# Optimization experiments

Measured on AMD Instinct MI355X. Metric: run time of the kernel, lower is better.

Reference implementation:

```python
import jax, jax.numpy as jnp
import numpy as np
import math

DEPTH = 3
HID = 32


def _dense_adj(edge_index, n, dtype):
    # scatter edges into dense adjacency, drop self-loops (gcn_norm re-adds them)
    A = jnp.zeros((n, n), dtype).at[edge_index[0], edge_index[1]].add(1.0)
    return A * (1.0 - jnp.eye(n, dtype=dtype))


def _gcn(x, A, W, b):
    # GCNConv(improved=True): self-loop weight 2.0, symmetric deg normalization
    n = A.shape[0]
    Ah = A + 2.0 * jnp.eye(n, dtype=x.dtype)
    deg = Ah.sum(axis=1)
    d = jnp.where(deg > 0, jax.lax.rsqrt(deg), 0.0)
    An = d[:, None] * Ah * d[None, :]
    return An @ (x @ W) + b


def _augment(A):
    # GraphUNet.augment_adj: add self loops, A @ A, remove self loops
    n = A.shape[0]
    Ai = A + jnp.eye(n, dtype=A.dtype)
    A2 = Ai @ Ai
    return A2 * (1.0 - jnp.eye(n, dtype=A.dtype))


def _topk_pool(x, A, p, k):
    # TopKPooling: score = tanh(x.p/||p||), keep top-k, scale kept features
    score = jnp.tanh((x @ p) / jnp.linalg.norm(p))
    _, perm = jax.lax.top_k(score, k)
    xp = x[perm] * score[perm][:, None]
    Ap = A[perm][:, perm]
    return xp, Ap, perm


def _graph_unet(x, edge_index, Ws, bs, Us, ubs, ps):
    n = x.shape[0]
    ratios = [2000.0 / n, 0.5, 0.5]
    A = _dense_adj(edge_index, n, x.dtype)
    x = jax.nn.relu(_gcn(x, A, Ws[0], bs[0]))
    xs, As, perms = [x], [A], []
    for i in range(1, DEPTH + 1):
        A = _augment(A)
        k = math.ceil(ratios[i - 1] * x.shape[0])  # static shapes: 2000,1000,500
        x, A, perm = _topk_pool(x, A, ps[i - 1], k)
        x = jax.nn.relu(_gcn(x, A, Ws[i], bs[i]))
        if i < DEPTH:
            xs.append(x)
            As.append(A)
        perms.append(perm)
    for i in range(DEPTH):
        j = DEPTH - 1 - i
        res, A, perm = xs[j], As[j], perms[j]
        up = jnp.zeros_like(res).at[perm].set(x)
        x = _gcn(res + up, A, Us[i], ubs[i])
        if i < DEPTH - 1:
            x = jax.nn.relu(x)
    return x


def setup_inputs() -> dict:
    key = jax.random.key(0)
    N, F_IN, C, E = 4096, 1433, 16, 131072
    ks = jax.random.split(key, 20)
    inp = {
        "x": jax.random.normal(ks[0], (N, F_IN), jnp.float32),
        "edge_index": jax.random.randint(ks[1], (2, E), 0, N, jnp.int64),
    }
    inp["W0"] = jax.random.normal(ks[2], (F_IN, HID), jnp.float32) * 0.05
    inp["b0"] = jnp.zeros((HID,), jnp.float32)
    for i in range(1, 4):
        inp[f"W{i}"] = jax.random.normal(ks[2 + i], (HID, HID), jnp.float32) * 0.1
        inp[f"b{i}"] = jnp.zeros((HID,), jnp.float32)
    inp["U0"] = jax.random.normal(ks[6], (HID, HID), jnp.float32) * 0.1
    inp["c0"] = jnp.zeros((HID,), jnp.float32)
    inp["U1"] = jax.random.normal(ks[7], (HID, HID), jnp.float32) * 0.1
    inp["c1"] = jnp.zeros((HID,), jnp.float32)
    inp["U2"] = jax.random.normal(ks[8], (HID, C), jnp.float32) * 0.1
    inp["c2"] = jnp.zeros((C,), jnp.float32)
    # TopKPooling score vectors
    for i in range(3):
        inp[f"p{i}"] = jax.random.normal(ks[9 + i], (HID,), jnp.float32)
    return inp


def reference(x, edge_index, W0, b0, W1, b1, W2, b2, W3, b3,
              U0, c0, U1, c1, U2, c2, p0, p1, p2):
    # eval mode: dropout_adj and F.dropout are identity
    Ws = [W0, W1, W2, W3]
    bs = [b0, b1, b2, b3]
    Us = [U0, U1, U2]
    ubs = [c0, c1, c2]
    ps = [p0, p1, p2]
    out = _graph_unet(x, edge_index, Ws, bs, Us, ubs, ps)
    return jax.nn.log_softmax(out, axis=1)
```

## Files before the change

### kernel.cpp

```cpp
#include <hip/hip_runtime.h>
#include <math.h>
#include <stddef.h>

#define N0   4096
#define NE   131072
#define FIN  1433
#define HID  32
#define NCLS 16
#define KP1  2000
#define KP2  1000
#define KP3  500
#define RCH  512

typedef __attribute__((ext_vector_type(8))) short bf16x8;
typedef __attribute__((ext_vector_type(4))) float f32x4;


__global__ __launch_bounds__(256) void k_fill0_u32(unsigned* p, size_t n) {
    size_t i = (size_t)blockIdx.x * blockDim.x + threadIdx.x;
    size_t st = (size_t)gridDim.x * blockDim.x;
    for (; i < n; i += st) p[i] = 0u;
}

__global__ __launch_bounds__(256) void k_scatter2c(const int* ei, unsigned* A0w, unsigned* A0Tw, int* ecnt) {
    int e = blockIdx.x * blockDim.x + threadIdx.x;
    if (e >= NE) return;
    int r = ei[e], c = ei[NE + e];
    if (r == c) return;
    size_t idx = (size_t)r * N0 + c;
    atomicAdd(&A0w[idx >> 2], 1u << (8 * (idx & 3)));
    size_t idt = (size_t)c * N0 + r;
    atomicAdd(&A0Tw[idt >> 2], 1u << (8 * (idt & 3)));
    atomicAdd(&ecnt[r], 1);
}

__global__ __launch_bounds__(256) void k_dvec(const int* ecnt, float* dv, int n) {
    int i = blockIdx.x * blockDim.x + threadIdx.x;
    if (i < n) dv[i] = (float)(1.0 / sqrt((double)ecnt[i] + 2.0));
}

__global__ __launch_bounds__(256) void k_scan1(const int* __restrict__ d, int* __restrict__ o) {
    __shared__ int buf[N0];
    __shared__ int part[256];
    int tid = threadIdx.x;
    for (int t = tid; t < N0; t += 256) buf[t] = d[t];
    __syncthreads();
    int base = tid * (N0 / 256);
    int s = 0;
    #pragma unroll
    for (int j = 0; j < N0 / 256; j++) s += buf[base + j];
    part[tid] = s;
    __syncthreads();
    for (int offd = 1; offd < 256; offd <<= 1) {
        int v = (tid >= offd) ? part[tid - offd] : 0;
        __syncthreads();
        part[tid] += v;
        __syncthreads();
    }
    int run = (tid == 0) ? 0 : part[tid - 1];
    #pragma unroll
    for (int j = 0; j < N0 / 256; j++) {
        int tmp = buf[base + j];
        o[base + j] = run;
        run += tmp;
    }
}

__global__ __launch_bounds__(256) void k_fillout(const int* ei, const int* outoff, int* ocur, int* outlist) {
    int e = blockIdx.x * 256 + threadIdx.x;
    if (e >= NE) return;
    int u = ei[e], v = ei[NE + e];
    if (u == v) return;
    int s = atomicAdd(&ocur[u], 1);
    outlist[outoff[u] + s] = v;
}

__global__ __launch_bounds__(256) void k_fcount(const int* ei, const int* rk, int* focnt) {
    int e = blockIdx.x * 256 + threadIdx.x;
    if (e >= NE) return;
    int u = ei[e], v = ei[NE + e];
    if (u == v) return;
    if (rk[v] < KP1) atomicAdd(&focnt[u], 1);
}

__global__ __launch_bounds__(256) void k_ffill(const int* ei, const int* rk, const int* foutoff,
                                               int* fcur, int* foutlist) {
    int e = blockIdx.x * 256 + threadIdx.x;
    if (e >= NE) return;
    int u = ei[e], v = ei[NE + e];
    if (u == v) return;
    int rv = rk[v];
    if (rv >= KP1) return;
    int s = atomicAdd(&fcur[u], 1);
    foutlist[foutoff[u] + s] = rv;
}

__global__ __launch_bounds__(256) void k_spaug2(const int* __restrict__ ecnt, const int* __restrict__ outoff,
                                                const int* __restrict__ outlist,
                                                const int* __restrict__ focnt, const int* __restrict__ foutoff,
                                                const int* __restrict__ foutlist,
                                                const int* __restrict__ perm,
                                                float* __restrict__ A1, float* __restrict__ dv1) {
    __shared__ float rowacc[KP1];
    __shared__ float red[256];
    int r1 = blockIdx.x, tid = threadIdx.x;
    for (int j = tid; j < KP1; j += 256) rowacc[j] = 0.f;
    int pr1 = perm[r1];
    __syncthreads();
    int od = ecnt[pr1], ob = outoff[pr1];
    for (int ki = tid; ki < od; ki += 256) {
        int k = outlist[ob + ki];
        int fb = foutoff[k], fc = focnt[k];
        for (int j = 0; j < fc; j++) atomicAdd(&rowacc[foutlist[fb + j]], 1.f);
    }
    {
        int fb = foutoff[pr1], fc = focnt[pr1];
        for (int j = tid; j < fc; j += 256) atomicAdd(&rowacc[foutlist[fb + j]], 2.f);
    }
    __syncthreads();
    if (tid == 0) rowacc[r1] = 0.f;
    __syncthreads();
    float rs = 0.f;
    for (int j = tid * 4; j < KP1; j += 1024) {
        float4 v = *(const float4*)&rowacc[j];
        rs += v.x + v.y + v.z + v.w;
        *(float4*)&A1[(size_t)r1 * KP1 + j] = v;
    }
    red[tid] = rs; __syncthreads();
    for (int o = 128; o > 0; o >>= 1) {
        if (tid < o) red[tid] += red[tid + o];
        __syncthreads();
    }
    if (tid == 0) dv1[r1] = (float)(1.0 / sqrt((double)red[0] + 2.0));
}

__global__ __launch_bounds__(256) void k_degf(const float* A, int n, float* dv) {
    int i = blockIdx.x;
    const float* row = A + (size_t)i * n;
    float acc = 0.f;
    for (int j = threadIdx.x * 4; j < n; j += 256 * 4) {
        float4 w = *(const float4*)&row[j];
        acc += w.x + w.y + w.z + w.w;
    }
    __shared__ float red[256];
    red[threadIdx.x] = acc; __syncthreads();
    for (int off = 128; off > 0; off >>= 1) {
        if (threadIdx.x < off) red[threadIdx.x] += red[threadIdx.x + off];
        __syncthreads();
    }
    if (threadIdx.x == 0) dv[i] = (float)(1.0 / sqrt((double)red[0] + 2.0));
}

template <int NC>
__global__ __launch_bounds__(256) void k_xw2(const float* __restrict__ X, const float* __restrict__ W,
                                             const float* __restrict__ dvv, float* __restrict__ YB,
                                             int M, int K,
                                             const float* __restrict__ UP, const int* __restrict__ rkl, int kup) {
    constexpr int BR = 256 / NC;
    constexpr int BK = 64;
    constexpr int XEL = BR * BK / 256;
    constexpr int WEL = BK * NC / 256;
    __shared__ float Xs[BR][BK + 4];
    __shared__ float Ws[BK][NC];
    int r0 = blockIdx.x * BR;
    int tid = threadIdx.x;
    int c = tid % NC, r = tid / NC;
    int xli = tid * XEL, xr = xli / BK, xc = xli % BK;
    int wli = tid * WEL, wk = wli / NC, wc = wli % NC;
    int grow = r0 + xr;
    int upr = -1;
    if (UP && grow < M) { int rr = rkl[grow]; if (rr < kup) upr = rr; }
    float acc = 0.f;

    for (int k0 = 0; k0 < K; k0 += BK) {
        __syncthreads();
        #pragma unroll
        for (int e = 0; e < XEL; e++) {
            int kk = k0 + xc + e;
            float v = (grow < M && kk < K) ? X[(size_t)grow * K + kk] : 0.f;
            if (upr >= 0 && kk < K) v += UP[(size_t)upr * K + kk];
            Xs[xr][xc + e] = v;
        }
        if (k0 + wk < K) {
            #pragma unroll
            for (int e = 0; e < WEL; e += 4)
                *(float4*)&Ws[wk][wc + e] = *(const float4*)&W[(size_t)(k0 + wk) * NC + wc + e];
        } else {
            #pragma unroll
            for (int e = 0; e < WEL; e++) Ws[wk][wc + e] = 0.f;
        }
        __syncthreads();
        #pragma unroll 8
        for (int k = 0; k < BK; k++) acc += Xs[r][k] * Ws[k][c];
    }
    int orow = r0 + r;
    if (orow < M) YB[(size_t)orow * NC + c] = dvv[orow] * acc;
}

__global__ __launch_bounds__(256) void k_xw2sk(const float* __restrict__ X, const float* __restrict__ W,
                                               float* __restrict__ xwp, int M, int K, int chunk) {
    constexpr int NC = 32, BR = 8, BK = 64;
    __shared__ float Xs[BR][BK + 4];
    __shared__ float Ws[BK][NC];
    int r0 = blockIdx.x * BR;
    int s  = blockIdx.y;
    int kb = s * chunk, ke = min(kb + chunk, K);
    int tid = threadIdx.x;
    int c = tid % NC, r = tid / NC;
    int xli = tid * 2, xr = xli / BK, xc = xli % BK;
    int wli = tid * 8, wk = wli / NC, wc = wli % NC;
    int grow = r0 + xr;
    float acc = 0.f;

    for (int k0 = kb; k0 < ke; k0 += BK) {
        __syncthreads();
        #pragma unroll
        for (int e = 0; e < 2; e++) {
            int kk = k0 + xc + e;
            Xs[xr][xc + e] = (grow < M && kk < K) ? X[(size_t)grow * K + kk] : 0.f;
        }
        if (k0 + wk < K) {
            #pragma unroll
            for (int e = 0; e < 8; e += 4)
                *(float4*)&Ws[wk][wc + e] = *(const float4*)&W[(size_t)(k0 + wk) * NC + wc + e];
        } else {
            #pragma unroll
            for (int e = 0; e < 8; e++) Ws[wk][wc + e] = 0.f;
        }
        __syncthreads();
        #pragma unroll 8
        for (int k = 0; k < BK; k++) acc += Xs[r][k] * Ws[k][c];
    }
    int orow = r0 + r;
    if (orow < M) xwp[((size_t)s * M + orow) * NC + c] = acc;
}

__global__ __launch_bounds__(256) void k_xwred(const float* __restrict__ xwp, int S,
                                               const float* __restrict__ dvv, float* __restrict__ yb, int M) {
    int idx = blockIdx.x * 256 + threadIdx.x;
    if (idx >= M * 32) return;
    float s = 0.f;
    for (int t = 0; t < S; t++) s += xwp[(size_t)t * M * 32 + idx];
    yb[idx] = dvv[idx / 32] * s;
}


template <class T, int NC>
__global__ __launch_bounds__(256) void k_agg(const T* __restrict__ A, const float* __restrict__ y,
                                             float* __restrict__ part, int n, int M, int chunk) {
    constexpr int G   = 256 / NC;
    constexpr int RPT = 64 / G;
    __shared__ float At[64][72];
    __shared__ float ys[64][NC];
    int r0 = blockIdx.x * 64;
    int s  = blockIdx.y;
    int k_begin = s * chunk;
    int k_end   = min(k_begin + chunk, n);
    int tid = threadIdx.x;
    int c = tid % NC, g = tid / NC;
    int r = tid & 63, kq = tid >> 6;
    bool row_ok = (r0 + r) < M;
    float acc[RPT] = {};

    for (int k0 = k_begin; k0 < k_end; k0 += 64) {
        __syncthreads();
        if constexpr (sizeof(T) == 1) {
            uint4 w = {0u, 0u, 0u, 0u};
            if (row_ok) w = *(const uint4*)&A[(size_t)(r0 + r) * n + k0 + kq * 16];
            #pragma unroll
            for (int j = 0; j < 16; j++) {
                int kl = kq * 16 + j;
                unsigned b = (((const unsigned*)&w)[j >> 2] >> (8 * (j & 3))) & 0xffu;
                At[kl][r] = (k0 + kl < k_end) ? (float)b : 0.f;
            }
        } else {
            #pragma unroll
            for (int q = 0; q < 4; q++) {
                int kl = kq * 16 + q * 4;
                float4 w = {0.f, 0.f, 0.f, 0.f};
                if (row_ok) w = *(const float4*)&A[(size_t)(r0 + r) * n + k0 + kl];
                At[kl + 0][r] = (k0 + kl + 0 < k_end) ? w.x : 0.f;
                At[kl + 1][r] = (k0 + kl + 1 < k_end) ? w.y : 0.f;
                At[kl + 2][r] = (k0 + kl + 2 < k_end) ? w.z : 0.f;
                At[kl + 3][r] = (k0 + kl + 3 < k_end) ? w.w : 0.f;
            }
        }
        constexpr int NF4 = 64 * NC / 4;
        #pragma unroll
        for (int f = 0; f < NF4 / 256; f++) {
            int fi = tid + f * 256;
            int k = fi / (NC / 4), cb = fi % (NC / 4);
            float4 w = *(const float4*)&y[(size_t)(k0 + k) * NC + cb * 4];
            *(float4*)&ys[k][cb * 4] = w;
        }
        __syncthreads();
        for (int k = 0; k < 64; k++) {
            float yv = ys[k][c];
            #pragma unroll
            for (int i = 0; i < RPT; i += 4) {
                float4 a = *(const float4*)&At[k][g * RPT + i];
                acc[i + 0] += a.x * yv;
                acc[i + 1] += a.y * yv;
                acc[i + 2] += a.z * yv;
                acc[i + 3] += a.w * yv;
            }
        }
    }
    #pragma unroll
    for (int i = 0; i < RPT; i++) {
        int row = r0 + g * RPT + i;
        if (row < M) part[((size_t)s * M + row) * NC + c] = acc[i];
    }
}

template <int NC>
__global__ __launch_bounds__(256) void k_aggfin(const float* __restrict__ part, int S,
                                                const float* __restrict__ y, const float* __restrict__ dvv,
                                                const float* __restrict__ bias, float* __restrict__ out,
                                                int M, int relu) {
    int idx = blockIdx.x * blockDim.x + threadIdx.x;
    if (idx >= M * NC) return;
    int i = idx / NC, c = idx % NC;
    float sum = 0.f;
    for (int s = 0; s < S; s++) sum += part[(size_t)s * M * NC + idx];
    float di = dvv[i];
    float v = di * sum + 2.f * di * y[idx] + bias[c];
    if (relu) v = fmaxf(v, 0.f);
    out[idx] = v;
}

__global__ __launch_bounds__(256) void k_aggfin_lsm(const float* __restrict__ part, int S,
                                                    const float* __restrict__ y, const float* __restrict__ dvv,
                                                    const float* __restrict__ bias, float* __restrict__ out,
                                                    int M) {
    __shared__ float vv[16][NCLS + 1];
    int idx = blockIdx.x * 256 + threadIdx.x;
    int i = idx / NCLS, c = idx % NCLS;
    int lr = threadIdx.x / NCLS;
    float v = 0.f;
    if (i < M) {
        float sum = 0.f;
        for (int s = 0; s < S; s++) sum += part[(size_t)s * M * NCLS + idx];
        float di = dvv[i];
        v = di * sum + 2.f * di * y[idx] + bias[c];
    }
    vv[lr][c] = v;
    __syncthreads();
    if (i >= M) return;
    float m = -1e30f;
    for (int cc = 0; cc < NCLS; cc++) m = fmaxf(m, vv[lr][cc]);
    float se = 0.f;
    for (int cc = 0; cc < NCLS; cc++) se += expf(vv[lr][cc] - m);
    float ls = logf(se);
    out[idx] = v - m - ls;
}


__global__ __launch_bounds__(256) void k_rankscore(const float* __restrict__ x, const float* __restrict__ p,
                                                   int* __restrict__ rk, int n) {
    __shared__ float sj[RCH];
    float pv[HID];
    #pragma unroll
    for (int c = 0; c < HID; c++) pv[c] = p[c];
    float nrm = 0.f;
    #pragma unroll
    for (int c = 0; c < HID; c++) nrm += pv[c] * pv[c];
    nrm = sqrtf(nrm);
    int jb = blockIdx.y * RCH;
    int len = min(jb + RCH, n) - jb;
    for (int t = threadIdx.x; t < len; t += 256) {
        const float* xr = x + (size_t)(jb + t) * HID;
        float d = 0.f;
        #pragma unroll
        for (int c = 0; c < HID; c++) d += xr[c] * pv[c];
        sj[t] = tanhf(d / nrm);
    }
    __syncthreads();
    int i = blockIdx.x * 256 + threadIdx.x;
    if (i >= n) return;
    const float* xi = x + (size_t)i * HID;
    float di = 0.f;
    #pragma unroll
    for (int c = 0; c < HID; c++) di += xi[c] * pv[c];
    float si = tanhf(di / nrm);
    int r = 0;
    for (int j = 0; j < len; j += 4) {
        float4 v = *(const float4*)&sj[j];
        int jg = jb + j;
        r += (v.x > si) || (v.x == si && (jg + 0) < i);
        r += (v.y > si) || (v.y == si && (jg + 1) < i);
        r += (v.z > si) || (v.z == si && (jg + 2) < i);
        r += (v.w > si) || (v.w == si && (jg + 3) < i);
    }
    atomicAdd(&rk[i], r);
}

__global__ __launch_bounds__(256) void k_permpool2(const float* __restrict__ x, const float* __restrict__ p,
                                                   const int* __restrict__ rk, int* __restrict__ perm,
                                                   float* __restrict__ xp, int n, int k) {
    int i = blockIdx.x * 256 + threadIdx.x;
    if (i >= n) return;
    int r = rk[i];
    if (r >= k) return;
    perm[r] = i;
    float pv[HID];
    #pragma unroll
    for (int c = 0; c < HID; c++) pv[c] = p[c];
    float nrm = 0.f;
    #pragma unroll
    for (int c = 0; c < HID; c++) nrm += pv[c] * pv[c];
    nrm = sqrtf(nrm);
    const float* xi = x + (size_t)i * HID;
    float d = 0.f;
    #pragma unroll
    for (int c = 0; c < HID; c++) d += xi[c] * pv[c];
    float si = tanhf(d / nrm);
    const float4* xr = (const float4*)xi;
    float4* xpo = (float4*)(xp + (size_t)r * HID);
    #pragma unroll
    for (int c = 0; c < HID / 4; c++) {
        float4 v = xr[c];
        v.x *= si; v.y *= si; v.z *= si; v.w *= si;
        xpo[c] = v;
    }
}


template <class T>
__global__ __launch_bounds__(256) void k_gcols(const T* A, const int* perm, T* CG, int n, int kk) {
    size_t idx = (size_t)blockIdx.x * blockDim.x + threadIdx.x;
    if (idx >= (size_t)n * kk) return;
    int k = (int)(idx / kk), r2 = (int)(idx % kk);
    int pc = perm[r2];
    T v = A[(size_t)k * n + pc];
    if (k == pc) v = (T)(v + (T)1);
    CG[idx] = v;
}

__global__ __launch_bounds__(256) void k_gemm_pool_sk(const float* A, const int* perm, const float* CG,
                                                      float* part, int n, int kk, int chunk) {
    __shared__ float As[16][65];
    __shared__ float Bs[16][65];
    __shared__ int   pr[64];
    int r0 = blockIdx.y * 64, c0 = blockIdx.x * 64;
    int s  = blockIdx.z;
    int k_begin = s * chunk;
    int k_end   = min(k_begin + chunk, n);
    int tx = threadIdx.x % 16, ty = threadIdx.x / 16;

    for (int t = threadIdx.x; t < 64; t += 256) {
        int rg = r0 + t;
        pr[t] = (rg < kk) ? perm[rg] : -1;
    }
    __syncthreads();

    float acc[4][4] = {};
    int cB = threadIdx.x % 64, kB = threadIdx.x / 64;

    for (int k0 = k_begin; k0 < k_end; k0 += 16) {
        for (int pass = 0; pass < 4; pass++) {
            int rr = ty + pass * 16;
            int kk_ = k0 + tx;
            int prow = pr[rr];
            float v = 0.f;
            if (prow >= 0 && kk_ < k_end) {
                v = A[(size_t)prow * n + kk_];
                if (prow == kk_) v += 1.f;
            }
            As[tx][rr] = v;
        }
        for (int pass = 0; pass < 4; pass++) {
            int k = kB + 4 * pass;
            int cg = c0 + cB;
            float v = 0.f;
            if (cg < kk && (k0 + k) < k_end) v = CG[(size_t)(k0 + k) * kk + cg];
            Bs[k][cB] = v;
        }
        __syncthreads();
        for (int k = 0; k < 16; k++) {
            float a[4], b[4];
            #pragma unroll
            for (int i = 0; i < 4; i++) a[i] = As[k][ty * 4 + i];
            #pragma unroll
            for (int j = 0; j < 4; j++) b[j] = Bs[k][tx * 4 + j];
            #pragma unroll
            for (int i = 0; i < 4; i++)
                #pragma unroll
                for (int j = 0; j < 4; j++) acc[i][j] += a[i] * b[j];
        }
        __syncthreads();
    }
    for (int i = 0; i < 4; i++) {
        int rg = r0 + ty * 4 + i;
        if (rg >= kk) continue;
        for (int j = 0; j < 4; j++) {
            int cg = c0 + tx * 4 + j;
            if (cg >= kk) continue;
            part[((size_t)s * kk + rg) * kk + cg] = acc[i][j];
        }
    }
}

__global__ __launch_bounds__(256) void k_gpfin(const float* __restrict__ part, int S, float* __restrict__ Ap, int kk) {
    int idx = blockIdx.x * blockDim.x + threadIdx.x;
    if (idx >= kk * kk) return;
    int rg = idx / kk, cg = idx % kk;
    float sum = 0.f;
    for (int s = 0; s < S; s++) sum += part[(size_t)s * kk * kk + idx];
    Ap[idx] = (rg == cg) ? 0.f : sum;
}


__global__ __launch_bounds__(256) void k_tr_f32(const float* A, float* AT, int n) {
    __shared__ float t[32][33];
    int bx = blockIdx.x * 32, by = blockIdx.y * 32;
    int tx = threadIdx.x % 32, ty = threadIdx.x / 32;
    for (int p = 0; p < 4; p++) {
        int r = by + ty + p * 8, c = bx + tx;
        t[ty + p * 8][tx] = (r < n && c < n) ? A[(size_t)r * n + c] : 0.f;
    }
    __syncthreads();
    for (int p = 0; p < 4; p++) {
        int r = bx + ty + p * 8, c = by + tx;
        if (r < n && c < n) AT[(size_t)r * n + c] = t[tx][ty + p * 8];
    }
}

__global__ __launch_bounds__(256) void k_prepfb(const float* A, const float* AT,
                                                int n, int Kpad, const int* perm, int kk,
                                                unsigned short* dstA, unsigned short* dstB) {
    const float* src = blockIdx.y ? AT : A;
    unsigned short* dst = blockIdx.y ? dstB : dstA;
    int r = blockIdx.x;
    unsigned short* drow = dst + (size_t)r * Kpad;
    if (r >= kk) {
        for (int k = threadIdx.x; k < Kpad; k += 256) drow[k] = 0;
        return;
    }
    int pr = perm[r];
    const float* srow = src + (size_t)pr * n;
    for (int k = threadIdx.x; k < Kpad; k += 256) {
        float v = (k < n) ? srow[k] : 0.f;
        if (k == pr) v += 1.f;
        drow[k] = (unsigned short)(__float_as_uint(v) >> 16);
    }
}

__global__ __launch_bounds__(512) void k_mfma_pool(const unsigned short* Abf, const unsigned short* Bbf,
                                                   float* Ap, int Kpad, int kk, int chunk) {
    __shared__ short As[128 * 64];
    __shared__ short Bs[128 * 64];
    int r0 = blockIdx.y * 128, c0 = blockIdx.x * 128;
    int z0 = blockIdx.z * chunk;
    int tid = threadIdx.x;
    int l = tid & 63, w = tid >> 6;
    int wm = w >> 2, wn = w & 3;
    f32x4 acc[4][2] = {};

    for (int k0 = z0; k0 < z0 + chunk; k0 += 64) {
        __syncthreads();
        #pragma unroll
        for (int p = 0; p < 2; p++) {
            int row = p * 64 + (tid >> 3);
            int ch  = tid & 7;
            int byte = row * 128 + ((ch * 16) ^ ((row & 7) << 4));
            bf16x8 va = *(const bf16x8*)&Abf[(size_t)(r0 + row) * Kpad + k0 + ch * 8];
            *(bf16x8*)((char*)As + byte) = va;
            bf16x8 vb = *(const bf16x8*)&Bbf[(size_t)(c0 + row) * Kpad + k0 + ch * 8];
            *(bf16x8*)((char*)Bs + byte) = vb;
        }
        __syncthreads();
        #pragma unroll
        for (int h = 0; h < 2; h++) {
            bf16x8 af[4], bfr[2];
            #pragma unroll
            for (int i = 0; i < 4; i++) {
                int row = wm * 64 + i * 16 + (l & 15);
                int byte = row * 128 + ((h * 64 + (l >> 4) * 16) ^ ((row & 7) << 4));
                af[i] = *(const bf16x8*)((const char*)As + byte);
            }
            #pragma unroll
            for (int j = 0; j < 2; j++) {
                int row = wn * 32 + j * 16 + (l & 15);
                int byte = row * 128 + ((h * 64 + (l >> 4) * 16) ^ ((row & 7) << 4));
                bfr[j] = *(const bf16x8*)((const char*)Bs + byte);
            }
            #pragma unroll
            for (int i = 0; i < 4; i++)
                #pragma unroll
                for (int j = 0; j < 2; j++)
                    acc[i][j] = __builtin_amdgcn_mfma_f32_16x16x32_bf16(af[i], bfr[j], acc[i][j], 0, 0, 0);
        }
    }
    #pragma unroll
    for (int i = 0; i < 4; i++) {
        #pragma unroll
        for (int j = 0; j < 2; j++) {
            int cg = c0 + wn * 32 + j * 16 + (l & 15);
            if (cg < kk) {
                #pragma unroll
                for (int q = 0; q < 4; q++) {
                    int rg = r0 + wm * 64 + i * 16 + (l >> 4) * 4 + q;
                    if (rg < kk && rg != cg) atomicAdd(&Ap[(size_t)rg * kk + cg], acc[i][j][q]);
                }
            }
        }
    }
}


extern "C" void kernel_launch(void* const* d_in, const int* in_sizes, int n_in,
                              void* d_out, int out_size, void* d_ws, size_t ws_size,
                              hipStream_t stream) {
    const float* x  = (const float*)d_in[0];
    const int*   ei = (const int*)d_in[1];
    const float* W0 = (const float*)d_in[2];  const float* b0 = (const float*)d_in[3];
    const float* W1 = (const float*)d_in[4];  const float* b1 = (const float*)d_in[5];
    const float* W2 = (const float*)d_in[6];  const float* b2 = (const float*)d_in[7];
    const float* W3 = (const float*)d_in[8];  const float* b3 = (const float*)d_in[9];
    const float* U0 = (const float*)d_in[10]; const float* c0 = (const float*)d_in[11];
    const float* U1 = (const float*)d_in[12]; const float* c1 = (const float*)d_in[13];
    const float* U2 = (const float*)d_in[14]; const float* c2 = (const float*)d_in[15];
    const float* p0 = (const float*)d_in[16];
    const float* p1 = (const float*)d_in[17];
    const float* p2 = (const float*)d_in[18];
    float* out = (float*)d_out;

    char* w = (char*)d_ws;
    size_t off = 0;
    auto alloc = [&](size_t bytes) -> void* {
        void* p = w + off;
        off += (bytes + 255) / 256 * 256;
        return p;
    };
    unsigned char* A0u = (unsigned char*)alloc((size_t)N0 * N0);
    unsigned char* A0T = (unsigned char*)alloc((size_t)N0 * N0);
    int*   ecnt = (int*)alloc((size_t)N0 * 4);
    int*   ocur = (int*)alloc((size_t)N0 * 4);
    int*   focnt = (int*)alloc((size_t)N0 * 4);
    int*   fcur  = (int*)alloc((size_t)N0 * 4);
    float* A1  = (float*)alloc((size_t)KP1 * KP1 * 4);
    float* A1T = (float*)alloc((size_t)KP1 * KP1 * 4);
    float* A2  = (float*)alloc((size_t)KP2 * KP2 * 4);
    float* A3  = (float*)alloc((size_t)KP3 * KP3 * 4);
    float* CG  = (float*)alloc((size_t)KP2 * KP3 * 4);
    unsigned short* Abf = (unsigned short*)alloc((size_t)2048 * 4096 * 2);
    unsigned short* Bbf = (unsigned short*)alloc((size_t)2048 * 4096 * 2);
    float* part = (float*)alloc((size_t)4 * N0 * HID * 4);
    float* x0  = (float*)alloc((size_t)N0 * HID * 4);
    float* x1  = (float*)alloc((size_t)KP1 * HID * 4);
    float* x2  = (float*)alloc((size_t)KP2 * HID * 4);
    float* x3  = (float*)alloc((size_t)KP3 * HID * 4);
    float* xp  = (float*)alloc((size_t)KP1 * HID * 4);
    float* ua  = (float*)alloc((size_t)KP2 * HID * 4);
    float* ub  = (float*)alloc((size_t)KP1 * HID * 4);
    float* yb  = (float*)alloc((size_t)N0 * HID * 4);
    float* dv0 = (float*)alloc((size_t)N0 * 4);
    float* dv1 = (float*)alloc((size_t)KP1 * 4);
    float* dv2 = (float*)alloc((size_t)KP2 * 4);
    float* dv3 = (float*)alloc((size_t)KP3 * 4);
    int*   rkA = (int*)alloc((size_t)N0 * 4);
    int*   rkB = (int*)alloc((size_t)KP1 * 4);
    int*   rkC = (int*)alloc((size_t)KP2 * 4);
    int*   pm0 = (int*)alloc((size_t)KP1 * 4);
    int*   pm1 = (int*)alloc((size_t)KP2 * 4);
    int*   pm2 = (int*)alloc((size_t)KP3 * 4);
    int*   outoff  = (int*)alloc((size_t)N0 * 4);
    int*   foutoff = (int*)alloc((size_t)N0 * 4);
    int*   outlist  = (int*)alloc((size_t)NE * 4);
    int*   foutlist = (int*)alloc((size_t)NE * 4);
    (void)ws_size; (void)in_sizes; (void)n_in; (void)out_size;

    auto gcn_f = [&](const float* A, int n, const float* xin, int K, const float* W,
                     const float* bias, const float* dvv, int relu, float* outv, int S, int chunk,
                     const float* UP, const int* rkl, int kup) {
        k_xw2<32><<<(n + 7) / 8, 256, 0, stream>>>(xin, W, dvv, yb, n, K, UP, rkl, kup);
        dim3 g((n + 63) / 64, S);
        k_agg<float, 32><<<g, 256, 0, stream>>>(A, yb, part, n, n, chunk);
        k_aggfin<32><<<(n * 32 + 255) / 256, 256, 0, stream>>>(part, S, yb, dvv, bias, outv, n, relu);
    };
    auto pool = [&](const float* xin, const float* p, int n, int k, int* rkbuf, int* perm, float* xpo) {
        k_fill0_u32<<<16, 256, 0, stream>>>((unsigned*)rkbuf, (size_t)n);
        dim3 gr((n + 255) / 256, (n + RCH - 1) / RCH);
        k_rankscore<<<gr, 256, 0, stream>>>(xin, p, rkbuf, n);
        k_permpool2<<<(n + 255) / 256, 256, 0, stream>>>(xin, p, rkbuf, perm, xpo, n, k);
    };

    k_fill0_u32<<<2048, 256, 0, stream>>>((unsigned*)A0u, ((size_t)2 * N0 * N0 + (size_t)4 * N0 * 4) / 4);
    k_scatter2c<<<(NE + 255) / 256, 256, 0, stream>>>(ei, (unsigned*)A0u, (unsigned*)A0T, ecnt);
    k_dvec<<<16, 256, 0, stream>>>(ecnt, dv0, N0);
    k_scan1<<<1, 256, 0, stream>>>(ecnt, outoff);
    k_fillout<<<(NE + 255) / 256, 256, 0, stream>>>(ei, outoff, ocur, outlist);

    k_xw2sk<<<dim3(N0 / 8, 4), 256, 0, stream>>>(x, W0, part, N0, FIN, 384);
    k_xwred<<<(N0 * 32 + 255) / 256, 256, 0, stream>>>(part, 4, dv0, yb, N0);
    {
        dim3 g((N0 + 63) / 64, 4);
        k_agg<unsigned char, 32><<<g, 256, 0, stream>>>(A0u, yb, part, N0, N0, 1024);
        k_aggfin<32><<<(N0 * 32 + 255) / 256, 256, 0, stream>>>(part, 4, yb, dv0, b0, x0, N0, 1);
    }
    pool(x0, p0, N0, KP1, rkA, pm0, xp);

    k_fcount<<<(NE + 255) / 256, 256, 0, stream>>>(ei, rkA, focnt);
    k_scan1<<<1, 256, 0, stream>>>(focnt, foutoff);
    k_ffill<<<(NE + 255) / 256, 256, 0, stream>>>(ei, rkA, foutoff, fcur, foutlist);
    k_spaug2<<<KP1, 256, 0, stream>>>(ecnt, outoff, outlist, focnt, foutoff, foutlist, pm0, A1, dv1);

    gcn_f(A1, KP1, xp, HID, W1, b1, dv1, 1, x1, 8, 256, nullptr, nullptr, 0);
    k_tr_f32<<<dim3(63, 63), 256, 0, stream>>>(A1, A1T, KP1);
    pool(x1, p1, KP1, KP2, rkB, pm1, xp);

    k_prepfb<<<dim3(1024, 2), 256, 0, stream>>>(A1, A1T, KP1, 2048, pm1, KP2, Abf, Bbf);
    k_fill0_u32<<<2048, 256, 0, stream>>>((unsigned*)A2, (size_t)KP2 * KP2);
    k_mfma_pool<<<dim3(8, 8, 4), 512, 0, stream>>>(Abf, Bbf, A2, 2048, KP2, 512);

    k_degf<<<KP2, 256, 0, stream>>>(A2, KP2, dv2);
    gcn_f(A2, KP2, xp, HID, W2, b2, dv2, 1, x2, 16, 64, nullptr, nullptr, 0);
    pool(x2, p2, KP2, KP3, rkC, pm2, xp);

    {
        size_t tot = (size_t)KP2 * KP3;
        k_gcols<float><<<(int)((tot + 255) / 256), 256, 0, stream>>>(A2, pm2, CG, KP2, KP3);
        float* pbuf = (float*)Abf;
        k_gemm_pool_sk<<<dim3(8, 8, 16), 256, 0, stream>>>(A2, pm2, CG, pbuf, KP2, KP3, 64);
        k_gpfin<<<(KP3 * KP3 + 255) / 256, 256, 0, stream>>>(pbuf, 16, A3, KP3);
    }
    k_degf<<<KP3, 256, 0, stream>>>(A3, KP3, dv3);
    gcn_f(A3, KP3, xp, HID, W3, b3, dv3, 1, x3, 8, 64, nullptr, nullptr, 0);

    gcn_f(A2, KP2, x2, HID, U0, c0, dv2, 1, ua, 16, 64, x3, rkC, KP3);
    gcn_f(A1, KP1, x1, HID, U1, c1, dv1, 1, ub, 8, 256, ua, rkB, KP2);

    k_xw2<16><<<(N0 + 15) / 16, 256, 0, stream>>>(x0, U2, dv0, yb, N0, HID, ub, rkA, KP1);
    {
        dim3 g((N0 + 63) / 64, 4);
        k_agg<unsigned char, 16><<<g, 256, 0, stream>>>(A0u, yb, part, N0, N0, 1024);
        k_aggfin_lsm<<<(N0 * NCLS) / 256, 256, 0, stream>>>(part, 4, yb, dv0, c2, out, N0);
    }
}
```

Baseline: 460.1 us.

## Replace dense level-0 adjacency aggregation with CSR sparse gather kernel

Drops the dense byte-packed 4096x4096 adjacency and its transpose at the top graph level. Both level-0 GCN aggregations (first down layer and final up layer) now gather neighbour features directly from the existing CSR out-lists, one block per row. The bias, ReLU and log-softmax epilogues are fused into that kernel. This removes the large zero-fill, the atomic scatter into the dense matrix, and the two dense passes over 16M entries. The cost is irregular gathers and a per-row block launch that may be underused on low-degree rows.

```diff
diff --git a/kernel.cpp b/kernel.cpp
--- a/kernel.cpp
+++ b/kernel.cpp
@@ -22,15 +22,11 @@
     for (; i < n; i += st) p[i] = 0u;
 }
 
-__global__ __launch_bounds__(256) void k_scatter2c(const int* ei, unsigned* A0w, unsigned* A0Tw, int* ecnt) {
+__global__ __launch_bounds__(256) void k_scatcnt(const int* ei, int* ecnt) {
     int e = blockIdx.x * blockDim.x + threadIdx.x;
     if (e >= NE) return;
     int r = ei[e], c = ei[NE + e];
     if (r == c) return;
-    size_t idx = (size_t)r * N0 + c;
-    atomicAdd(&A0w[idx >> 2], 1u << (8 * (idx & 3)));
-    size_t idt = (size_t)c * N0 + r;
-    atomicAdd(&A0Tw[idt >> 2], 1u << (8 * (idt & 3)));
     atomicAdd(&ecnt[r], 1);
 }
 
@@ -132,6 +128,47 @@
         __syncthreads();
     }
     if (tid == 0) dv1[r1] = (float)(1.0 / sqrt((double)red[0] + 2.0));
+}
+
+template <int NC, int MODE>
+__global__ __launch_bounds__(256) void k_spagg(const int* __restrict__ outoff, const int* __restrict__ ecnt,
+                                               const int* __restrict__ outlist,
+                                               const float* __restrict__ y, const float* __restrict__ dvv,
+                                               const float* __restrict__ bias, float* __restrict__ outp) {
+    constexpr int G = 256 / NC;
+    __shared__ float red[256];
+    __shared__ float fin[NC];
+    int i = blockIdx.x;
+    int tid = threadIdx.x;
+    int c = tid % NC, g = tid / NC;
+    int od = ecnt[i], ob = outoff[i];
+    float acc = 0.f;
+    for (int j = g; j < od; j += G)
+        acc += y[(size_t)outlist[ob + j] * NC + c];
+    red[tid] = acc;
+    __syncthreads();
+    for (int o = G / 2; o > 0; o >>= 1) {
+        if (g < o) red[tid] += red[tid + o * NC];
+        __syncthreads();
+    }
+    if (tid < NC) {
+        float di = dvv[i];
+        float v = di * red[tid] + 2.f * di * y[(size_t)i * NC + tid] + bias[tid];
+        if (MODE == 0) v = fmaxf(v, 0.f);
+        fin[tid] = v;
+    }
+    __syncthreads();
+    if (tid < NC) {
+        if (MODE == 2) {
+            float m = -1e30f;
+            for (int cc = 0; cc < NC; cc++) m = fmaxf(m, fin[cc]);
+            float se = 0.f;
+            for (int cc = 0; cc < NC; cc++) se += expf(fin[cc] - m);
+            outp[(size_t)i * NC + tid] = fin[tid] - m - logf(se);
+        } else {
+            outp[(size_t)i * NC + tid] = fin[tid];
+        }
+    }
 }
 
 __global__ __launch_bounds__(256) void k_degf(const float* A, int n, float* dv) {
@@ -264,26 +301,15 @@
 
     for (int k0 = k_begin; k0 < k_end; k0 += 64) {
         __syncthreads();
-        if constexpr (sizeof(T) == 1) {
-            uint4 w = {0u, 0u, 0u, 0u};
-            if (row_ok) w = *(const uint4*)&A[(size_t)(r0 + r) * n + k0 + kq * 16];
-            #pragma unroll
-            for (int j = 0; j < 16; j++) {
-                int kl = kq * 16 + j;
-                unsigned b = (((const unsigned*)&w)[j >> 2] >> (8 * (j & 3))) & 0xffu;
-                At[kl][r] = (k0 + kl < k_end) ? (float)b : 0.f;
-            }
-        } else {
-            #pragma unroll
-            for (int q = 0; q < 4; q++) {
-                int kl = kq * 16 + q * 4;
-                float4 w = {0.f, 0.f, 0.f, 0.f};
-                if (row_ok) w = *(const float4*)&A[(size_t)(r0 + r) * n + k0 + kl];
-                At[kl + 0][r] = (k0 + kl + 0 < k_end) ? w.x : 0.f;
-                At[kl + 1][r] = (k0 + kl + 1 < k_end) ? w.y : 0.f;
-                At[kl + 2][r] = (k0 + kl + 2 < k_end) ? w.z : 0.f;
-                At[kl + 3][r] = (k0 + kl + 3 < k_end) ? w.w : 0.f;
-            }
+        #pragma unroll
+        for (int q = 0; q < 4; q++) {
+            int kl = kq * 16 + q * 4;
+            float4 w = {0.f, 0.f, 0.f, 0.f};
+            if (row_ok) w = *(const float4*)&A[(size_t)(r0 + r) * n + k0 + kl];
+            At[kl + 0][r] = (k0 + kl + 0 < k_end) ? w.x : 0.f;
+            At[kl + 1][r] = (k0 + kl + 1 < k_end) ? w.y : 0.f;
+            At[kl + 2][r] = (k0 + kl + 2 < k_end) ? w.z : 0.f;
+            At[kl + 3][r] = (k0 + kl + 3 < k_end) ? w.w : 0.f;
         }
         constexpr int NF4 = 64 * NC / 4;
         #pragma unroll
@@ -327,32 +353,6 @@
     float v = di * sum + 2.f * di * y[idx] + bias[c];
     if (relu) v = fmaxf(v, 0.f);
     out[idx] = v;
-}
-
-__global__ __launch_bounds__(256) void k_aggfin_lsm(const float* __restrict__ part, int S,
-                                                    const float* __restrict__ y, const float* __restrict__ dvv,
-                                                    const float* __restrict__ bias, float* __restrict__ out,
-                                                    int M) {
-    __shared__ float vv[16][NCLS + 1];
-    int idx = blockIdx.x * 256 + threadIdx.x;
-    int i = idx / NCLS, c = idx % NCLS;
-    int lr = threadIdx.x / NCLS;
-    float v = 0.f;
-    if (i < M) {
-        float sum = 0.f;
-        for (int s = 0; s < S; s++) sum += part[(size_t)s * M * NCLS + idx];
-        float di = dvv[i];
-        v = di * sum + 2.f * di * y[idx] + bias[c];
-    }
-    vv[lr][c] = v;
-    __syncthreads();
-    if (i >= M) return;
-    float m = -1e30f;
-    for (int cc = 0; cc < NCLS; cc++) m = fmaxf(m, vv[lr][cc]);
-    float se = 0.f;
-    for (int cc = 0; cc < NCLS; cc++) se += expf(vv[lr][cc] - m);
-    float ls = logf(se);
-    out[idx] = v - m - ls;
 }
 
 
@@ -633,8 +633,6 @@
         off += (bytes + 255) / 256 * 256;
         return p;
     };
-    unsigned char* A0u = (unsigned char*)alloc((size_t)N0 * N0);
-    unsigned char* A0T = (unsigned char*)alloc((size_t)N0 * N0);
     int*   ecnt = (int*)alloc((size_t)N0 * 4);
     int*   ocur = (int*)alloc((size_t)N0 * 4);
     int*   focnt = (int*)alloc((size_t)N0 * 4);
@@ -686,19 +684,15 @@
         k_permpool2<<<(n + 255) / 256, 256, 0, stream>>>(xin, p, rkbuf, perm, xpo, n, k);
     };
 
-    k_fill0_u32<<<2048, 256, 0, stream>>>((unsigned*)A0u, ((size_t)2 * N0 * N0 + (size_t)4 * N0 * 4) / 4);
-    k_scatter2c<<<(NE + 255) / 256, 256, 0, stream>>>(ei, (unsigned*)A0u, (unsigned*)A0T, ecnt);
+    k_fill0_u32<<<16, 256, 0, stream>>>((unsigned*)ecnt, (size_t)4 * N0);
+    k_scatcnt<<<(NE + 255) / 256, 256, 0, stream>>>(ei, ecnt);
     k_dvec<<<16, 256, 0, stream>>>(ecnt, dv0, N0);
     k_scan1<<<1, 256, 0, stream>>>(ecnt, outoff);
     k_fillout<<<(NE + 255) / 256, 256, 0, stream>>>(ei, outoff, ocur, outlist);
 
     k_xw2sk<<<dim3(N0 / 8, 4), 256, 0, stream>>>(x, W0, part, N0, FIN, 384);
     k_xwred<<<(N0 * 32 + 255) / 256, 256, 0, stream>>>(part, 4, dv0, yb, N0);
-    {
-        dim3 g((N0 + 63) / 64, 4);
-        k_agg<unsigned char, 32><<<g, 256, 0, stream>>>(A0u, yb, part, N0, N0, 1024);
-        k_aggfin<32><<<(N0 * 32 + 255) / 256, 256, 0, stream>>>(part, 4, yb, dv0, b0, x0, N0, 1);
-    }
+    k_spagg<32, 0><<<N0, 256, 0, stream>>>(outoff, ecnt, outlist, yb, dv0, b0, x0);
     pool(x0, p0, N0, KP1, rkA, pm0, xp);
 
     k_fcount<<<(NE + 255) / 256, 256, 0, stream>>>(ei, rkA, focnt);
@@ -732,9 +726,5 @@
     gcn_f(A1, KP1, x1, HID, U1, c1, dv1, 1, ub, 8, 256, ua, rkB, KP2);
 
     k_xw2<16><<<(N0 + 15) / 16, 256, 0, stream>>>(x0, U2, dv0, yb, N0, HID, ub, rkA, KP1);
-    {
-        dim3 g((N0 + 63) / 64, 4);
-        k_agg<unsigned char, 16><<<g, 256, 0, stream>>>(A0u, yb, part, N0, N0, 1024);
-        k_aggfin_lsm<<<(N0 * NCLS) / 256, 256, 0, stream>>>(part, 4, yb, dv0, c2, out, N0);
-    }
-}
+    k_spagg<16, 2><<<N0, 256, 0, stream>>>(outoff, ecnt, outlist, yb, dv0, c2, out);
+}
```

After: 379.9 us. 1.21x faster.
